# Kernel optimization log

Hardware: AMD Instinct MI355X
Metric: run time of the kernel (lower is better)

Reference implementation:

```python
import jax, jax.numpy as jnp
import numpy as np

B, S, N, H, F, L, Lt = 2, 8, 150, 128, 40, 2, 1
EF = 2 * F + 2  # 82: src feat + dst feat + distance + bond
_rows_np, _cols_np = np.where(~np.eye(N, dtype=bool))  # fully connected, no self loops
_rows = jnp.asarray(_rows_np)
_cols = jnp.asarray(_cols_np)
E = _rows_np.shape[0]


def setup_inputs() -> dict:
    key = jax.random.key(0)
    ks = jax.random.split(key, 20)
    w = lambda k, shape: 0.1 * jax.random.normal(k, shape, dtype=jnp.float32)
    d = {}
    d['t'] = jax.random.uniform(ks[0], (B, 1), dtype=jnp.float32)
    d['x'] = jax.random.normal(ks[1], (B, S, N, 3), dtype=jnp.float32)
    d['peptide_seq'] = jax.random.randint(ks[2], (B, 15), 0, 20)
    d['atom_labels'] = jax.random.randint(ks[3], (B, N), 0, 5)
    d['amino_acid_pos'] = jax.random.randint(ks[4], (B, N), 1, 16)
    d['bond_matrix'] = (jax.random.uniform(ks[5], (B, N, N)) < 0.1).astype(jnp.float32)
    d['edge_mask'] = jnp.ones((B, N, N), jnp.float32)
    d['atom_mask'] = jnp.ones((B, N, 1), jnp.float32)
    d['restore_indices'] = jnp.tile(jnp.eye(N, dtype=jnp.float32)[None], (B, 1, 1))
    d['W_e1'] = w(ks[6], (L, EF, H)); d['b_e1'] = jnp.zeros((L, H), jnp.float32)
    d['W_e2'] = w(ks[7], (L, H, H)); d['b_e2'] = jnp.zeros((L, H), jnp.float32)
    d['W_c'] = w(ks[8], (L, H, 1)); d['b_c'] = jnp.zeros((L, 1), jnp.float32)
    d['W_h'] = w(ks[9], (L, F + H, F)); d['b_h'] = jnp.zeros((L, F), jnp.float32)
    d['w_t'] = w(ks[10], (L, 1, H)); d['w_b_t'] = jnp.zeros((L, H), jnp.float32)
    d['tW_e1'] = w(ks[11], (Lt, EF, H)); d['tb_e1'] = jnp.zeros((Lt, H), jnp.float32)
    d['tW_e2'] = w(ks[12], (Lt, H, H)); d['tb_e2'] = jnp.zeros((Lt, H), jnp.float32)
    d['tW_c'] = w(ks[13], (Lt, H, 1)); d['tb_c'] = jnp.zeros((Lt, 1), jnp.float32)
    d['tW_h'] = w(ks[14], (Lt, F + H, F)); d['tb_h'] = jnp.zeros((Lt, F), jnp.float32)
    return d


def _forward(t, x, peptide_seq, atom_labels, amino_acid_pos, bond_matrix, edge_mask,
             atom_mask, restore_indices, W_e1, b_e1, W_e2, b_e2, W_c, b_c, W_h, b_h,
             w_t, w_b_t, tW_e1, tb_e1, tW_e2, tb_e2, tW_c, tb_c, tW_h, tb_h):
    # single-atom embedding: [B, N, 40]
    aa = jnp.take_along_axis(peptide_seq, amino_acid_pos - 1, axis=1)
    emb = jnp.concatenate([
        jax.nn.one_hot(atom_labels, 5, dtype=x.dtype),
        jax.nn.one_hot(aa, 20, dtype=x.dtype),
        jax.nn.one_hot(amino_acid_pos - 1, 15, dtype=x.dtype)], axis=-1)
    h = jnp.broadcast_to(emb[:, None], (B, S, N, F))
    # restore absolute coordinates: x[b,s,i,d] = sum_j x[b,s,j,d] * R[b,i,j]
    x = jnp.einsum('bsjd,bij->bsid', x, restore_indices)
    x0 = x
    # per-edge masks/features (gathered once; identical math to full cdist + indexing)
    em_e = edge_mask.reshape(B, 1, N * N)[:, :, _rows * N + _cols][..., None]  # [B,1,E,1]
    bond_e = jnp.broadcast_to(bond_matrix[:, _rows, _cols][:, None, :, None], (B, S, E, 1))

    def layer(x, h, We1, be1, We2, be2, Wc, bc, Wh, bh, temb):
        diff = x[:, :, _rows] - x[:, :, _cols]                      # [B,S,E,3]
        dist = jnp.sqrt(jnp.sum(diff * diff, -1, keepdims=True) + 1e-12)
        ef = jnp.concatenate([h[:, :, _rows], h[:, :, _cols], dist, bond_e], -1)  # [B,S,E,82]
        m = jax.nn.silu(ef @ We1 + be1 + temb)
        m = jax.nn.silu(m @ We2 + be2) * em_e                        # [B,S,E,H]
        cw = m @ Wc + bc                                             # [B,S,E,1]
        x_out = jnp.zeros_like(x).at[:, :, _rows].add(diff * cw) / (N - 1)
        agg = jnp.zeros((B, S, N, m.shape[-1]), m.dtype).at[:, :, _rows].add(m)
        h_out = jax.nn.silu(jnp.concatenate([h, agg], -1) @ Wh + bh)
        return x_out, h_out

    for l in range(L):
        temb = (t @ w_t[l] + w_b_t[l])[:, None, None, :]             # [B,1,1,H]
        xo, h = layer(x, h, W_e1[l], b_e1[l], W_e2[l], b_e2[l], W_c[l], b_c[l], W_h[l], b_h[l], temb)
        x = x + xo
    for l in range(Lt):
        xo, h = layer(x, h, tW_e1[l], tb_e1[l], tW_e2[l], tb_e2[l], tW_c[l], tb_c[l], tW_h[l], tb_h[l], 0.0)
        x = x + xo
    return (x - x0) * atom_mask[:, None, :, :]


def reference(t, x, peptide_seq, atom_labels, amino_acid_pos, bond_matrix, edge_mask,
              atom_mask, restore_indices, W_e1, b_e1, W_e2, b_e2, W_c, b_c, W_h, b_h,
              w_t, w_b_t, tW_e1, tb_e1, tW_e2, tb_e2, tW_c, tb_c, tW_h, tb_h):
    return _forward(t, x, peptide_seq, atom_labels, amino_acid_pos, bond_matrix, edge_mask,
                    atom_mask, restore_indices, W_e1, b_e1, W_e2, b_e2, W_c, b_c, W_h, b_h,
                    w_t, w_b_t, tW_e1, tb_e1, tW_e2, tb_e2, tW_c, tb_c, tW_h, tb_h)
```

## Files before the change

### kernel.cpp

```cpp
#include <hip/hip_runtime.h>
#include <math.h>

#define B_ 2
#define S_ 8
#define N_ 150
#define H_ 128
#define F_ 40
#define EF_ 82
#define NP_ 160
#define MPQ 136
#define NB_ 2400

typedef __attribute__((ext_vector_type(8))) short short8;
typedef __attribute__((ext_vector_type(4))) float float4v;

__device__ __forceinline__ float silu_f(float v) {
    return v * __builtin_amdgcn_rcpf(1.0f + __expf(-v));
}

__device__ __forceinline__ unsigned short f2bf(float f) {
    unsigned u = __builtin_bit_cast(unsigned, f);
    return (unsigned short)((u + 0x7fffu + ((u >> 16) & 1u)) >> 16);
}

__device__ __forceinline__ unsigned cvt_pk_bf16(float lo, float hi) {
    unsigned r;
    asm("v_cvt_pk_bf16_f32 %0, %1, %2" : "=v"(r) : "v"(lo), "v"(hi));
    return r;
}

__global__ void prelude_kernel(const float* __restrict__ W_e2,
                               const float* __restrict__ tW_e2,
                               unsigned short* __restrict__ we2t,
                               const float* __restrict__ x,
                               const float* __restrict__ R,
                               float* __restrict__ xa,
                               float* __restrict__ x0,
                               const int* __restrict__ pep,
                               const int* __restrict__ labels,
                               const int* __restrict__ aapos,
                               const float* __restrict__ We1,
                               const float* __restrict__ be1,
                               const float* __restrict__ tp,
                               const float* __restrict__ wt,
                               const float* __restrict__ wbt,
                               float* __restrict__ h0,
                               float* __restrict__ Af,
                               float* __restrict__ Bf,
                               const float* __restrict__ W_h,
                               float* __restrict__ whT,
                               const float* __restrict__ We1L1,
                               const float* __restrict__ tWe1,
                               float* __restrict__ w1nT) {
    int bid = blockIdx.x;
    int tid = threadIdx.x;
    if (bid < 192) {
        int e = bid * 256 + tid;
        int l = e >> 14, idx = e & 16383;
        int k = idx >> 7, c = idx & 127;
        const float* src = (l == 0) ? W_e2 : (l == 1) ? (W_e2 + H_ * H_) : tW_e2;
        we2t[l * 16384 + c * H_ + k] = f2bf(src[idx]);
    } else if (bid < 221) {
        int idx = (bid - 192) * 256 + tid;
        if (idx < B_ * S_ * N_ * 3) {
            int d = idx % 3;
            int i = (idx / 3) % N_;
            int bs = idx / (3 * N_);
            int b = bs / S_;
            const float* xrow = x + bs * N_ * 3 + d;
            const float* Rrow = R + (b * N_ + i) * N_;
            float acc = 0.0f;
            for (int j = 0; j < N_; j++) acc += xrow[j * 3] * Rrow[j];
            xa[idx] = acc;
            x0[idx] = acc;
        }
    } else if (bid < 371) {
        int rel = bid - 221;
        int bi = rel * 2 + (tid >> 7);
        int b = bi / N_, i = bi % N_;
        int c = tid & 127;
        int al = labels[bi];
        int ap = aapos[bi];
        int aa = pep[b * 15 + ap - 1];
        int r0 = al, r1 = 5 + aa, r2 = 25 + ap - 1;
        float fa = We1[r0 * H_ + c] + We1[r1 * H_ + c] + We1[r2 * H_ + c]
                 + be1[c] + tp[b] * wt[c] + wbt[c];
        float fb = We1[(F_ + r0) * H_ + c] + We1[(F_ + r1) * H_ + c] + We1[(F_ + r2) * H_ + c];
        float hv = 0.0f;
        if (c < F_) hv = (c == r0 || c == r1 || c == r2) ? 1.0f : 0.0f;
        for (int s = 0; s < S_; s++) {
            int n = (b * S_ + s) * N_ + i;
            Af[n * H_ + c] = fa;
            Bf[n * H_ + c] = fb;
            if (c < F_) h0[n * F_ + c] = hv;
        }
    } else if (bid < 424) {
        int e = (bid - 371) * 256 + tid;
        if (e < 2 * F_ * 168) {
            int l = e / 6720, idx = e % 6720;
            int f = idx / 168, k = idx % 168;
            whT[l * 6720 + f * 168 + k] = W_h[l * 6720 + k * F_ + f];
        }
    } else {
        int e = (bid - 424) * 256 + tid;
        int s = e / 10240, idx = e % 10240;
        int c = idx / 80, k = idx % 80;
        const float* src = s ? tWe1 : We1L1;
        w1nT[s * 10240 + c * 80 + k] = src[k * H_ + c];
    }
}

__global__ __launch_bounds__(256, 4) void edge_fused_kernel(
    const float* __restrict__ x_in,
    const float* __restrict__ Afeat,
    const float* __restrict__ Bfeat,
    const float* __restrict__ We1,
    const unsigned short* __restrict__ we2t,
    const float* __restrict__ be2,
    const float* __restrict__ Wc,
    const float* __restrict__ bcp,
    const float* __restrict__ bond,
    const float* __restrict__ emask,
    const float* __restrict__ h_in,
    const float* __restrict__ whTp,
    const float* __restrict__ bh,
    const float* __restrict__ w1nTp,
    const float* __restrict__ be1n,
    const float* __restrict__ tp,
    const float* __restrict__ wtn,
    const float* __restrict__ wbtn,
    int has_t,
    const float* __restrict__ x0v,
    const float* __restrict__ amask,
    int final_mode,
    float* __restrict__ x_out,
    float* __restrict__ h_out,
    float* __restrict__ Af_out,
    float* __restrict__ Bf_out)
{
    __shared__ __align__(16) short mbuf[2][16 * MPQ];
    __shared__ float4 diffE[NP_];
    __shared__ float2 dbL[NP_];
    __shared__ float DsumL[3];
    __shared__ float wpart[4][3];
    __shared__ float catL[F_ + H_];
    __shared__ float partL[120];
    __shared__ float hnewL[F_];

    int blk = blockIdx.x;
    int i = blk % N_, bs = blk / N_, b = bs / S_;
    int tid = threadIdx.x;
    int node = bs * N_ + i;
    int lane = tid & 63, w = tid >> 6;
    int qd = lane >> 4, l15 = lane & 15;
    int rowLoc = tid >> 4, c0 = (tid & 15) * 8;

    float xi0 = x_in[node * 3 + 0];
    float xi1 = x_in[node * 3 + 1];
    float xi2 = x_in[node * 3 + 2];

    if (tid < NP_) {
        int j = tid;
        float xj0 = xi0, xj1 = xi1, xj2 = xi2, bnd = 0.0f, emv = 0.0f;
        if (j < N_) {
            int nj = bs * N_ + j;
            xj0 = x_in[nj * 3 + 0];
            xj1 = x_in[nj * 3 + 1];
            xj2 = x_in[nj * 3 + 2];
            int eij = (b * N_ + i) * N_ + j;
            bnd = bond[eij];
            emv = (j == i) ? 0.0f : emask[eij];
        }
        float d0 = xi0 - xj0, d1 = xi1 - xj1, d2 = xi2 - xj2;
        diffE[j] = make_float4(d0, d1, d2, emv);
        dbL[j] = make_float2(sqrtf(d0 * d0 + d1 * d1 + d2 * d2 + 1e-12f), bnd);
    }

    float afr[8], w80r[8], w81r[8];
    {
        float4 t0 = *(const float4*)&Afeat[node * H_ + c0];
        float4 t1 = *(const float4*)&Afeat[node * H_ + c0 + 4];
        afr[0]=t0.x; afr[1]=t0.y; afr[2]=t0.z; afr[3]=t0.w;
        afr[4]=t1.x; afr[5]=t1.y; afr[6]=t1.z; afr[7]=t1.w;
        t0 = *(const float4*)&We1[80 * H_ + c0];
        t1 = *(const float4*)&We1[80 * H_ + c0 + 4];
        w80r[0]=t0.x; w80r[1]=t0.y; w80r[2]=t0.z; w80r[3]=t0.w;
        w80r[4]=t1.x; w80r[5]=t1.y; w80r[6]=t1.z; w80r[7]=t1.w;
        t0 = *(const float4*)&We1[81 * H_ + c0];
        t1 = *(const float4*)&We1[81 * H_ + c0 + 4];
        w81r[0]=t0.x; w81r[1]=t0.y; w81r[2]=t0.z; w81r[3]=t0.w;
        w81r[4]=t1.x; w81r[5]=t1.y; w81r[6]=t1.z; w81r[7]=t1.w;
    }

    int ctb = w * 2;
    float b2r0 = be2[ctb * 16 + l15],  b2r1 = be2[ctb * 16 + 16 + l15];
    float wc0  = Wc[ctb * 16 + l15],   wc1  = Wc[ctb * 16 + 16 + l15];
    const unsigned short* bb0 = we2t + (ctb * 16 + l15) * H_ + qd * 8;
    const unsigned short* bb1 = bb0 + 16 * H_;
    short8 bf00 = *(const short8*)(bb0 +  0);
    short8 bf01 = *(const short8*)(bb0 + 32);
    short8 bf02 = *(const short8*)(bb0 + 64);
    short8 bf03 = *(const short8*)(bb0 + 96);
    short8 bf10 = *(const short8*)(bb1 +  0);
    short8 bf11 = *(const short8*)(bb1 + 32);
    short8 bf12 = *(const short8*)(bb1 + 64);
    short8 bf13 = *(const short8*)(bb1 + 96);

    __syncthreads();

    if (w == 0) {
        float p0 = 0, p1 = 0, p2 = 0;
        for (int j = lane; j < NP_; j += 64) {
            float4 d = diffE[j];
            p0 += d.x; p1 += d.y; p2 += d.z;
        }
        for (int s = 1; s < 64; s <<= 1) {
            p0 += __shfl_xor(p0, s, 64);
            p1 += __shfl_xor(p1, s, 64);
            p2 += __shfl_xor(p2, s, 64);
        }
        if (lane == 0) { DsumL[0] = p0; DsumL[1] = p1; DsumL[2] = p2; }
    }

    float aggP0 = 0, aggP1 = 0;
    float SP00 = 0, SP01 = 0, SP02 = 0, SP10 = 0, SP11 = 0, SP12 = 0;

    for (int jt = 0; jt < 10; jt++) {
        short* mb = mbuf[jt & 1];
        int jrow = jt * 16 + rowLoc;
        float mv[8];
        if (jrow < N_) {
            const float* bp = &Bfeat[(bs * N_ + jrow) * H_ + c0];
            float4 b0 = *(const float4*)bp;
            float4 b1 = *(const float4*)(bp + 4);
            float br[8] = {b0.x, b0.y, b0.z, b0.w, b1.x, b1.y, b1.z, b1.w};
            float2 db = dbL[jrow];
#pragma unroll
            for (int u = 0; u < 8; u++)
                mv[u] = silu_f(afr[u] + br[u] + db.x * w80r[u] + db.y * w81r[u]);
        } else {
#pragma unroll
            for (int u = 0; u < 8; u++) mv[u] = 0.0f;
        }
        uint4 pk;
        pk.x = cvt_pk_bf16(mv[0], mv[1]);
        pk.y = cvt_pk_bf16(mv[2], mv[3]);
        pk.z = cvt_pk_bf16(mv[4], mv[5]);
        pk.w = cvt_pk_bf16(mv[6], mv[7]);
        *(uint4*)&mb[rowLoc * MPQ + c0] = pk;
        __syncthreads();

        const short* arow = &mb[l15 * MPQ + qd * 8];
        short8 a0 = *(const short8*)(arow +  0);
        short8 a1 = *(const short8*)(arow + 32);
        short8 a2 = *(const short8*)(arow + 64);
        short8 a3 = *(const short8*)(arow + 96);
        float4v acc0 = {0, 0, 0, 0}, acc1 = {0, 0, 0, 0};
        acc0 = __builtin_amdgcn_mfma_f32_16x16x32_bf16(a0, bf00, acc0, 0, 0, 0);
        acc1 = __builtin_amdgcn_mfma_f32_16x16x32_bf16(a0, bf10, acc1, 0, 0, 0);
        acc0 = __builtin_amdgcn_mfma_f32_16x16x32_bf16(a1, bf01, acc0, 0, 0, 0);
        acc1 = __builtin_amdgcn_mfma_f32_16x16x32_bf16(a1, bf11, acc1, 0, 0, 0);
        acc0 = __builtin_amdgcn_mfma_f32_16x16x32_bf16(a2, bf02, acc0, 0, 0, 0);
        acc1 = __builtin_amdgcn_mfma_f32_16x16x32_bf16(a2, bf12, acc1, 0, 0, 0);
        acc0 = __builtin_amdgcn_mfma_f32_16x16x32_bf16(a3, bf03, acc0, 0, 0, 0);
        acc1 = __builtin_amdgcn_mfma_f32_16x16x32_bf16(a3, bf13, acc1, 0, 0, 0);

#pragma unroll
        for (int r = 0; r < 4; r++) {
            int j = jt * 16 + qd * 4 + r;
            float4 de = diffE[j];
            float mv0 = silu_f(acc0[r] + b2r0) * de.w;
            float mv1 = silu_f(acc1[r] + b2r1) * de.w;
            aggP0 += mv0; aggP1 += mv1;
            SP00 += de.x * mv0; SP01 += de.y * mv0; SP02 += de.z * mv0;
            SP10 += de.x * mv1; SP11 += de.y * mv1; SP12 += de.z * mv1;
        }
    }

#define QR_(v) { v += __shfl_xor(v, 16, 64); v += __shfl_xor(v, 32, 64); }
    QR_(aggP0) QR_(aggP1)
    QR_(SP00) QR_(SP01) QR_(SP02)
    QR_(SP10) QR_(SP11) QR_(SP12)
#undef QR_

    if (!final_mode) {
        if (qd == 0) {
            catL[F_ + ctb * 16 + l15]      = aggP0;
            catL[F_ + ctb * 16 + 16 + l15] = aggP1;
        }
        if (tid < F_) catL[tid] = h_in[node * F_ + tid];
    }

    float p0 = wc0 * SP00 + wc1 * SP10;
    float p1 = wc0 * SP01 + wc1 * SP11;
    float p2 = wc0 * SP02 + wc1 * SP12;
    for (int s = 1; s < 16; s <<= 1) {
        p0 += __shfl_xor(p0, s, 64);
        p1 += __shfl_xor(p1, s, 64);
        p2 += __shfl_xor(p2, s, 64);
    }
    if (lane == 0) { wpart[w][0] = p0; wpart[w][1] = p1; wpart[w][2] = p2; }
    __syncthreads();
    if (tid < 3) {
        float tot = wpart[0][tid] + wpart[1][tid] + wpart[2][tid] + wpart[3][tid]
                  + bcp[0] * DsumL[tid];
        float xn = x_in[node * 3 + tid] + tot * (1.0f / (float)(N_ - 1));
        if (final_mode)
            x_out[node * 3 + tid] = (xn - x0v[node * 3 + tid]) * amask[b * N_ + i];
        else
            x_out[node * 3 + tid] = xn;
    }

    if (final_mode) return;

    if (tid < 120) {
        int f = tid % 40, ks = tid / 40;
        int k0 = ks * 56;
        const float* wr = whTp + f * 168 + k0;
        float p = 0.0f;
#pragma unroll
        for (int k = 0; k < 56; k += 4) {
            float4 wv = *(const float4*)(wr + k);
            p += catL[k0 + k]     * wv.x;
            p += catL[k0 + k + 1] * wv.y;
            p += catL[k0 + k + 2] * wv.z;
            p += catL[k0 + k + 3] * wv.w;
        }
        partL[tid] = p;
    }
    __syncthreads();
    if (tid < F_) {
        float hv = silu_f(partL[tid] + partL[40 + tid] + partL[80 + tid] + bh[tid]);
        hnewL[tid] = hv;
        h_out[node * F_ + tid] = hv;
    }
    __syncthreads();
    {
        int c = tid & 127;
        int isB = tid >> 7;
        float acc = isB ? 0.0f
                        : (be1n[c] + (has_t ? tp[b] * wtn[c] + wbtn[c] : 0.0f));
        const float* wr = w1nTp + c * 80 + isB * 40;
#pragma unroll
        for (int k = 0; k < 40; k += 4) {
            float4 wv = *(const float4*)(wr + k);
            acc += hnewL[k]     * wv.x;
            acc += hnewL[k + 1] * wv.y;
            acc += hnewL[k + 2] * wv.z;
            acc += hnewL[k + 3] * wv.w;
        }
        (isB ? Bf_out : Af_out)[node * H_ + c] = acc;
    }
}

extern "C" void kernel_launch(void* const* d_in, const int* in_sizes, int n_in,
                              void* d_out, int out_size, void* d_ws, size_t ws_size,
                              hipStream_t stream) {
    const float* t     = (const float*)d_in[0];
    const float* x     = (const float*)d_in[1];
    const int*   pep   = (const int*)d_in[2];
    const int*   labels= (const int*)d_in[3];
    const int*   aapos = (const int*)d_in[4];
    const float* bond  = (const float*)d_in[5];
    const float* em    = (const float*)d_in[6];
    const float* amask = (const float*)d_in[7];
    const float* R     = (const float*)d_in[8];
    const float* W_e1  = (const float*)d_in[9];
    const float* b_e1  = (const float*)d_in[10];
    const float* W_e2  = (const float*)d_in[11];
    const float* b_e2  = (const float*)d_in[12];
    const float* W_c   = (const float*)d_in[13];
    const float* b_c   = (const float*)d_in[14];
    const float* W_h   = (const float*)d_in[15];
    const float* b_h   = (const float*)d_in[16];
    const float* w_t   = (const float*)d_in[17];
    const float* w_b_t = (const float*)d_in[18];
    const float* tW_e1 = (const float*)d_in[19];
    const float* tb_e1 = (const float*)d_in[20];
    const float* tW_e2 = (const float*)d_in[21];
    const float* tb_e2 = (const float*)d_in[22];
    const float* tW_c  = (const float*)d_in[23];
    const float* tb_c  = (const float*)d_in[24];
    float* out = (float*)d_out;

    float* ws = (float*)d_ws;
    unsigned short* we2t = (unsigned short*)ws;
    float* x0   = ws + 24576;
    float* xA   = x0 + 7200;
    float* xB   = xA + 7200;
    float* hA   = xB + 7200;
    float* hB   = hA + 96000;
    float* Af1  = hB + 96000;
    float* Bf1  = Af1 + 307200;
    float* Af2  = Bf1 + 307200;
    float* Bf2  = Af2 + 307200;
    float* whT  = Bf2 + 307200;
    float* w1nT = whT + 13440;

    prelude_kernel<<<504, 256, 0, stream>>>(W_e2, tW_e2, we2t, x, R, xA, x0,
                                            pep, labels, aapos, W_e1, b_e1,
                                            t, w_t, w_b_t, hA, Af1, Bf1,
                                            W_h, whT,
                                            W_e1 + EF_ * H_, tW_e1, w1nT);

    edge_fused_kernel<<<NB_, 256, 0, stream>>>(
        xA, Af1, Bf1, W_e1, we2t, b_e2, W_c, b_c, bond, em,
        hA, whT, b_h, w1nT, b_e1 + H_, t, w_t + H_, w_b_t + H_, 1,
        nullptr, nullptr, 0,
        xB, hB, Af2, Bf2);

    edge_fused_kernel<<<NB_, 256, 0, stream>>>(
        xB, Af2, Bf2, W_e1 + EF_ * H_, we2t + 16384, b_e2 + H_, W_c + H_, b_c + 1,
        bond, em,
        hB, whT + 6720, b_h + F_, w1nT + 10240, tb_e1, nullptr, nullptr, nullptr, 0,
        nullptr, nullptr, 0,
        xA, hA, Af1, Bf1);

    edge_fused_kernel<<<NB_, 256, 0, stream>>>(
        xA, Af1, Bf1, tW_e1, we2t + 32768, tb_e2, tW_c, tb_c, bond, em,
        nullptr, nullptr, nullptr, nullptr, nullptr, nullptr, nullptr, nullptr, 0,
        x0, amask, 1,
        out, nullptr, nullptr, nullptr);
}
```

Before: 265.2 us.

## Prefetch Bfeat tiles into LDS via async global_load_lds double buffering

Replaces the direct global loads of the neighbour Bfeat rows in the edge loop with asynchronous global-to-LDS copies into a swizzled, double-buffered shared tile. The next tile is issued right after the barrier so its fetch overlaps the MFMA work of the current tile. This adds 16 KB of LDS per block, which may lower occupancy, plus a vmcnt wait each iteration. The last tile reads past row 150 within the buffer (rows up to 160), which relies on the allocation being large enough.

```diff
diff --git a/kernel.cpp b/kernel.cpp
--- a/kernel.cpp
+++ b/kernel.cpp
@@ -27,6 +27,13 @@
     unsigned r;
     asm("v_cvt_pk_bf16_f32 %0, %1, %2" : "=v"(r) : "v"(lo), "v"(hi));
     return r;
+}
+
+__device__ __forceinline__ void g2lds16(const float* g, float* l) {
+    __builtin_amdgcn_global_load_lds(
+        (const __attribute__((address_space(1))) unsigned int*)g,
+        (__attribute__((address_space(3))) unsigned int*)l,
+        16, 0, 0);
 }
 
 __global__ void prelude_kernel(const float* __restrict__ W_e2,
@@ -139,6 +146,7 @@
     float* __restrict__ Bf_out)
 {
     __shared__ __align__(16) short mbuf[2][16 * MPQ];
+    __shared__ __align__(16) float bpref[2][2048];
     __shared__ float4 diffE[NP_];
     __shared__ float2 dbL[NP_];
     __shared__ float DsumL[3];
@@ -158,6 +166,18 @@
     float xi0 = x_in[node * 3 + 0];
     float xi1 = x_in[node * 3 + 1];
     float xi2 = x_in[node * 3 + 2];
+
+    const float* bbase = Bfeat + (size_t)(bs * N_) * H_;
+    int dI0 = (w * 2) * 64 + lane;
+    int dI1 = dI0 + 64;
+    int sOffA = (dI0 ^ ((dI0 >> 5) & 7)) << 2;
+    int sOffB = (dI1 ^ ((dI1 >> 5) & 7)) << 2;
+    int rdSlot = (rowLoc * 32 + (tid & 15) * 2) ^ (rowLoc & 7);
+    int rdOff0 = rdSlot << 2;
+    int rdOff1 = (rdSlot ^ 1) << 2;
+
+    g2lds16(bbase + sOffA, &bpref[0][w * 512]);
+    g2lds16(bbase + sOffB, &bpref[0][w * 512 + 256]);
 
     if (tid < NP_) {
         int j = tid;
@@ -227,12 +247,13 @@
 
     for (int jt = 0; jt < 10; jt++) {
         short* mb = mbuf[jt & 1];
+        const float* bp = bpref[jt & 1];
+        asm volatile("s_waitcnt vmcnt(0)" ::: "memory");
         int jrow = jt * 16 + rowLoc;
         float mv[8];
         if (jrow < N_) {
-            const float* bp = &Bfeat[(bs * N_ + jrow) * H_ + c0];
-            float4 b0 = *(const float4*)bp;
-            float4 b1 = *(const float4*)(bp + 4);
+            float4 b0 = *(const float4*)&bp[rdOff0];
+            float4 b1 = *(const float4*)&bp[rdOff1];
             float br[8] = {b0.x, b0.y, b0.z, b0.w, b1.x, b1.y, b1.z, b1.w};
             float2 db = dbL[jrow];
 #pragma unroll
@@ -249,6 +270,13 @@
         pk.w = cvt_pk_bf16(mv[6], mv[7]);
         *(uint4*)&mb[rowLoc * MPQ + c0] = pk;
         __syncthreads();
+
+        if (jt < 9) {
+            const float* nb = bbase + (jt + 1) * 2048;
+            float* pd = bpref[(jt + 1) & 1];
+            g2lds16(nb + sOffA, pd + w * 512);
+            g2lds16(nb + sOffB, pd + w * 512 + 256);
+        }
 
         const short* arow = &mb[l15 * MPQ + qd * 8];
         short8 a0 = *(const short8*)(arow +  0);
```

Result: no change. 265.8 us (+0.2%).
